# Performance work log

Hardware: AMD Instinct MI355X
Metric: run time of the kernel (lower is better)

## Reference

```python
import jax, jax.numpy as jnp
import numpy as np

B, C, L = 8, 256, 8192
H, D = 8, 64
INNER = H * D


def setup_inputs() -> dict:
    key = jax.random.key(0)
    ks = jax.random.split(key, 6)
    scale = 1.0 / np.sqrt(C)
    x = jax.random.normal(ks[0], (B, C, L), dtype=jnp.float32)
    Wq = jax.random.normal(ks[1], (INNER, C), dtype=jnp.float32) * scale
    Wk = jax.random.normal(ks[2], (INNER, C), dtype=jnp.float32) * scale
    Wv = jax.random.normal(ks[3], (INNER, C), dtype=jnp.float32) * scale
    Wo = jax.random.normal(ks[4], (C, INNER), dtype=jnp.float32) * (1.0 / np.sqrt(INNER))
    bo = jax.random.normal(ks[5], (C,), dtype=jnp.float32) * 0.01
    return {"x": x, "Wq": Wq, "Wk": Wk, "Wv": Wv, "Wo": Wo, "bo": bo}


def reference(x, Wq, Wk, Wv, Wo, bo):
    # 1x1 Conv1d == per-position matmul over channels: (inner,C) x (B,C,L) -> (B,inner,L)
    def proj(W):
        y = jnp.einsum('ic,bcl->bil', W, x)          # (B, inner, L)
        return y.reshape(B, H, D, L).transpose(0, 1, 3, 2)  # (B, H, L, D)

    q = jax.nn.softmax(proj(Wq), axis=-1)   # softmax over feature dim d
    k = jax.nn.softmax(proj(Wk), axis=-2)   # softmax over length dim L
    v = proj(Wv)

    context = jnp.einsum('bhld,bhlm->bhdm', k, v)   # (B, H, D, D)
    out = jnp.einsum('bhld,bhdm->bhlm', q, context) # (B, H, L, D)
    out = out.transpose(0, 1, 3, 2).reshape(B, INNER, L)  # (B, inner, L)
    return jnp.einsum('ci,bil->bcl', Wo, out) + bo[None, :, None]
```

## Files before the change

### kernel.cpp

```cpp
#include <hip/hip_runtime.h>

#define Bn 8
#define Cn 256
#define Ln 8192
#define Hn 8
#define Dn 64
#define IN 512
#define NSLAB 32

typedef __attribute__((ext_vector_type(4))) float f32x4;
typedef __attribute__((ext_vector_type(8))) __bf16 bf16x8;
typedef __attribute__((ext_vector_type(8))) unsigned short us8;

__device__ __forceinline__ float bf2f(unsigned short u) {
  unsigned int i = ((unsigned int)u) << 16;
  return __builtin_bit_cast(float, i);
}
__device__ __forceinline__ unsigned short f2bf(float f) {
  unsigned int i = __builtin_bit_cast(unsigned int, f);
  i += 0x7FFFu + ((i >> 16) & 1u);
  return (unsigned short)(i >> 16);
}
__device__ __forceinline__ bf16x8 asbf(us8 u) { return __builtin_bit_cast(bf16x8, u); }
__device__ __forceinline__ f32x4 mfma16(bf16x8 a, bf16x8 b, f32x4 c) {
  return __builtin_amdgcn_mfma_f32_16x16x32_bf16(a, b, c, 0, 0, 0);
}
__device__ __forceinline__ void gll16(const void* g, void* l) {
  __builtin_amdgcn_global_load_lds((const __attribute__((address_space(1))) void*)g,
                                   (__attribute__((address_space(3))) void*)l, 16, 0, 0);
}

__global__ __launch_bounds__(256) void k_xt(const float* __restrict__ x,
                                            unsigned short* __restrict__ xT) {
  __shared__ unsigned short tl[64 * 66];
  const int t = threadIdx.x;
  const int l0 = blockIdx.x * 64, c0 = blockIdx.y * 64, b = blockIdx.z;
#pragma unroll
  for (int it = 0; it < 4; ++it) {
    int lin = it * 256 + t;
    int c = lin >> 4;
    int l4 = (lin & 15) * 4;
    const float* gp = x + ((size_t)(b * Cn + c0 + c) * Ln + l0 + l4);
    f32x4 v = *(const f32x4*)gp;
    unsigned int p0 = (unsigned int)f2bf(v[0]) | ((unsigned int)f2bf(v[1]) << 16);
    unsigned int p1 = (unsigned int)f2bf(v[2]) | ((unsigned int)f2bf(v[3]) << 16);
    unsigned int* d = (unsigned int*)&tl[c * 66 + l4];
    d[0] = p0;
    d[1] = p1;
  }
  __syncthreads();
#pragma unroll
  for (int it = 0; it < 2; ++it) {
    int lin = it * 256 + t;
    int l = lin >> 3;
    int s = lin & 7;
    unsigned short v[8];
#pragma unroll
    for (int j = 0; j < 8; ++j) v[j] = tl[(s * 8 + j) * 66 + l];
    uint4 pk;
    pk.x = (unsigned)v[0] | ((unsigned)v[1] << 16);
    pk.y = (unsigned)v[2] | ((unsigned)v[3] << 16);
    pk.z = (unsigned)v[4] | ((unsigned)v[5] << 16);
    pk.w = (unsigned)v[6] | ((unsigned)v[7] << 16);
    *(uint4*)&xT[(size_t)(b * Ln + l0 + l) * Cn + c0 + s * 8] = pk;
  }
}

__global__ __launch_bounds__(256) void k_wcv(const float* __restrict__ Wq, const float* __restrict__ Wk,
                                             const float* __restrict__ Wv, const float* __restrict__ Wo,
                                             unsigned short* __restrict__ Wqkv,
                                             unsigned short* __restrict__ Wob) {
  int i = (blockIdx.x * 256 + threadIdx.x) * 4;
  const float* s;
  unsigned short* d;
  if (i < 393216) {
    int p = i >> 17;
    int w = i & 131071;
    s = (p == 0 ? Wq : (p == 1 ? Wk : Wv)) + w;
    d = Wqkv + i;
  } else {
    int w = i - 393216;
    s = Wo + w;
    d = Wob + w;
  }
  f32x4 v = *(const f32x4*)s;
  uint2 pk;
  pk.x = (unsigned)f2bf(v[0]) | ((unsigned)f2bf(v[1]) << 16);
  pk.y = (unsigned)f2bf(v[2]) | ((unsigned)f2bf(v[3]) << 16);
  *(uint2*)d = pk;
}

__global__ __launch_bounds__(256) void k_projq(const unsigned short* __restrict__ xT,
                                               const unsigned short* __restrict__ Wqkv,
                                               unsigned short* __restrict__ SqT) {
  __shared__ unsigned short lds[18432];
  const int tid = threadIdx.x, lane = tid & 63, wave = tid >> 6;
  const int lr = lane & 15, lg = lane >> 4;
  const int n0 = blockIdx.x * 128, m0 = blockIdx.y * 128, b = blockIdx.z;
  const int wm = (wave >> 1) * 64, wn = (wave & 1) * 64;
  unsigned short* Wt = lds;
  unsigned short* Xt = lds + 8192;

  f32x4 zero = {0.f, 0.f, 0.f, 0.f};
  f32x4 acc[4][4];
#pragma unroll
  for (int mt = 0; mt < 4; ++mt)
#pragma unroll
    for (int nt = 0; nt < 4; ++nt) acc[mt][nt] = zero;

  const int sr = tid >> 3, sc = (tid & 7) * 8;
  const unsigned short* wsrc = Wqkv + (size_t)(m0 + sr) * Cn + sc;
  const unsigned short* xsrc = xT + (size_t)(b * Ln + n0 + sr) * Cn + sc;

  for (int kt = 0; kt < 4; ++kt) {
    const int k0 = kt * 64;
#pragma unroll
    for (int it = 0; it < 4; ++it) {
      gll16(wsrc + (size_t)(it * 32) * Cn + k0, Wt + it * 2048 + tid * 8);
      gll16(xsrc + (size_t)(it * 32) * Cn + k0, Xt + it * 2048 + tid * 8);
    }
    __syncthreads();
#pragma unroll
    for (int ks = 0; ks < 2; ++ks) {
      const int kc = ks * 32 + lg * 8;
      bf16x8 af[4], bfv[4];
#pragma unroll
      for (int mt = 0; mt < 4; ++mt)
        af[mt] = asbf(*(const us8*)(Wt + (wm + mt * 16 + lr) * 64 + kc));
#pragma unroll
      for (int nt = 0; nt < 4; ++nt)
        bfv[nt] = asbf(*(const us8*)(Xt + (wn + nt * 16 + lr) * 64 + kc));
#pragma unroll
      for (int mt = 0; mt < 4; ++mt)
#pragma unroll
        for (int nt = 0; nt < 4; ++nt) acc[mt][nt] = mfma16(af[mt], bfv[nt], acc[mt][nt]);
    }
    __syncthreads();
  }

  unsigned short* T = lds + wave * 4608;
#pragma unroll
  for (int mt = 0; mt < 4; ++mt)
#pragma unroll
    for (int nt = 0; nt < 4; ++nt) {
      int ll = nt * 16 + lr, ii = mt * 16 + lg * 4;
      uint2 pk;
      pk.x = (unsigned)f2bf(acc[mt][nt][0]) | ((unsigned)f2bf(acc[mt][nt][1]) << 16);
      pk.y = (unsigned)f2bf(acc[mt][nt][2]) | ((unsigned)f2bf(acc[mt][nt][3]) << 16);
      *(uint2*)&T[ll * 72 + ii] = pk;
    }
  __syncthreads();
#pragma unroll
  for (int p = 0; p < 8; ++p) {
    int ll = p * 8 + (lane >> 3), s = lane & 7;
    uint4 v = *(const uint4*)&T[ll * 72 + s * 8];
    *(uint4*)&SqT[(size_t)(b * Ln + n0 + wn + ll) * IN + m0 + wm + s * 8] = v;
  }
}

__global__ __launch_bounds__(256) void k_projkv(const unsigned short* __restrict__ xT,
                                                const unsigned short* __restrict__ Wqkv,
                                                float* __restrict__ ctxP,
                                                float* __restrict__ den) {
  __shared__ unsigned short lds[17408];
  unsigned short* Wt = lds;
  unsigned short* Xt = lds + 8192;
  unsigned short* ek = lds;
  unsigned short* vt = lds + 64 * 136;
  const int tid = threadIdx.x, lane = tid & 63, wave = tid >> 6;
  const int lr = lane & 15, lg = lane >> 4;
  const int h = blockIdx.y, b = blockIdx.z;
  const int l0 = blockIdx.x * 256;
  const int wm = (wave >> 1) * 64, wn = (wave & 1) * 64;
  const int sr = tid >> 3, sc = (tid & 7) * 8;
  f32x4 zero = {0.f, 0.f, 0.f, 0.f};

  f32x4 cacc[4];
  cacc[0] = zero; cacc[1] = zero; cacc[2] = zero; cacc[3] = zero;
  float dacc[4][4] = {};

  for (int sub = 0; sub < 2; ++sub) {
    const int ls = l0 + sub * 128;
    f32x4 acc[4][4];
#pragma unroll
    for (int mt = 0; mt < 4; ++mt)
#pragma unroll
      for (int nt = 0; nt < 4; ++nt) acc[mt][nt] = zero;

    const unsigned short* xsrc = xT + (size_t)(b * Ln + ls + sr) * Cn + sc;
    for (int kt = 0; kt < 4; ++kt) {
      const int k0 = kt * 64;
#pragma unroll
      for (int it = 0; it < 4; ++it) {
        int gr = (it < 2 ? 512 : 960) + h * 64 + it * 32 + sr;
        gll16(Wqkv + (size_t)gr * Cn + k0 + sc, Wt + it * 2048 + tid * 8);
        gll16(xsrc + (size_t)(it * 32) * Cn + k0, Xt + it * 2048 + tid * 8);
      }
      __syncthreads();
#pragma unroll
      for (int ks = 0; ks < 2; ++ks) {
        const int kc = ks * 32 + lg * 8;
        bf16x8 af[4], bfv[4];
#pragma unroll
        for (int mt = 0; mt < 4; ++mt)
          af[mt] = asbf(*(const us8*)(Wt + (wm + mt * 16 + lr) * 64 + kc));
#pragma unroll
        for (int nt = 0; nt < 4; ++nt)
          bfv[nt] = asbf(*(const us8*)(Xt + (wn + nt * 16 + lr) * 64 + kc));
#pragma unroll
        for (int mt = 0; mt < 4; ++mt)
#pragma unroll
          for (int nt = 0; nt < 4; ++nt) acc[mt][nt] = mfma16(af[mt], bfv[nt], acc[mt][nt]);
      }
      __syncthreads();
    }

    if (wave < 2) {
#pragma unroll
      for (int mt = 0; mt < 4; ++mt)
#pragma unroll
        for (int nt = 0; nt < 4; ++nt) {
          int lcol = wn + nt * 16 + lr;
#pragma unroll
          for (int r = 0; r < 4; ++r) {
            float e = __expf(acc[mt][nt][r]);
            dacc[mt][r] += e;
            ek[(mt * 16 + lg * 4 + r) * 136 + lcol] = f2bf(e);
          }
        }
    } else {
#pragma unroll
      for (int mt = 0; mt < 4; ++mt)
#pragma unroll
        for (int nt = 0; nt < 4; ++nt) {
          int lcol = wn + nt * 16 + lr;
#pragma unroll
          for (int r = 0; r < 4; ++r)
            vt[(mt * 16 + lg * 4 + r) * 136 + lcol] = f2bf(acc[mt][nt][r]);
        }
    }
    __syncthreads();

    const int mq = wave * 16;
#pragma unroll
    for (int ks = 0; ks < 4; ++ks) {
      const int kc = ks * 32 + lg * 8;
      bf16x8 a = asbf(*(const us8*)(vt + (mq + lr) * 136 + kc));
#pragma unroll
      for (int dt = 0; dt < 4; ++dt) {
        bf16x8 bb = asbf(*(const us8*)(ek + (dt * 16 + lr) * 136 + kc));
        cacc[dt] = mfma16(a, bb, cacc[dt]);
      }
    }
    __syncthreads();
  }

  if (wave < 2) {
#pragma unroll
    for (int mt = 0; mt < 4; ++mt)
#pragma unroll
      for (int r = 0; r < 4; ++r) {
        float v = dacc[mt][r];
        v += __shfl_xor(v, 1);
        v += __shfl_xor(v, 2);
        v += __shfl_xor(v, 4);
        v += __shfl_xor(v, 8);
        if (lr == 0) atomicAdd(&den[(b * Hn + h) * 64 + mt * 16 + lg * 4 + r], v);
      }
  }
  float* cb = ctxP + ((size_t)blockIdx.x * 64 + b * Hn + h) * 4096;
  const int mq = wave * 16;
#pragma unroll
  for (int dt = 0; dt < 4; ++dt)
#pragma unroll
    for (int r = 0; r < 4; ++r)
      cb[(mq + lg * 4 + r) * 64 + dt * 16 + lr] = cacc[dt][r];
}

__global__ __launch_bounds__(256) void k_nrm(const float* __restrict__ ctxP,
                                             const float* __restrict__ den,
                                             unsigned short* __restrict__ ctxb) {
  const int bh = blockIdx.x, mz = blockIdx.y, t = threadIdx.x;
  const int m = mz * 16 + (t >> 4), dc = (t & 15) * 4;
  const float* base = ctxP + (size_t)bh * 4096 + m * 64 + dc;
  f32x4 s = {0.f, 0.f, 0.f, 0.f};
  for (int sl = 0; sl < NSLAB; ++sl) {
    f32x4 v = *(const f32x4*)(base + (size_t)sl * 64 * 4096);
    s += v;
  }
  f32x4 d4 = *(const f32x4*)(den + bh * 64 + dc);
  uint2 pk;
  pk.x = (unsigned)f2bf(s[0] / d4[0]) | ((unsigned)f2bf(s[1] / d4[1]) << 16);
  pk.y = (unsigned)f2bf(s[2] / d4[2]) | ((unsigned)f2bf(s[3] / d4[3]) << 16);
  *(uint2*)(ctxb + (size_t)bh * 4096 + m * 64 + dc) = pk;
}

__global__ __launch_bounds__(256) void k_out(const unsigned short* __restrict__ SqT,
                                             const unsigned short* __restrict__ ctxb,
                                             const unsigned short* __restrict__ Wob,
                                             const float* __restrict__ bo,
                                             float* __restrict__ out) {
  __shared__ unsigned short ot[64 * 256];
  const int tid = threadIdx.x, lane = tid & 63, w = tid >> 6;
  const int lr = lane & 15, lg = lane >> 4;
  const int l0 = blockIdx.x * 64, b = blockIdx.y;
  f32x4 zero = {0.f, 0.f, 0.f, 0.f};

  f32x4 acc[4][4];
#pragma unroll
  for (int mt = 0; mt < 4; ++mt)
#pragma unroll
    for (int nt = 0; nt < 4; ++nt) acc[mt][nt] = zero;

  const unsigned short* qb = SqT + (size_t)(b * Ln + l0 + w * 16 + lr) * IN + lg * 8;
  us8 r0 = *(const us8*)qb;
  us8 r1 = *(const us8*)(qb + 32);
  for (int half = 0; half < 2; ++half) {
#pragma unroll
    for (int hh = 0; hh < 4; ++hh) {
      const int h = half * 4 + hh;
      us8 n0, n1;
      if (h < 7) {
        n0 = *(const us8*)(qb + (h + 1) * 64);
        n1 = *(const us8*)(qb + (h + 1) * 64 + 32);
      }
      float qv[16];
#pragma unroll
      for (int j = 0; j < 8; ++j) {
        qv[j] = bf2f(r0[j]);
        qv[8 + j] = bf2f(r1[j]);
      }
      float mx = qv[0];
#pragma unroll
      for (int j = 1; j < 16; ++j) mx = fmaxf(mx, qv[j]);
      mx = fmaxf(mx, __shfl_xor(mx, 16));
      mx = fmaxf(mx, __shfl_xor(mx, 32));
      float sm = 0.f;
#pragma unroll
      for (int j = 0; j < 16; ++j) {
        qv[j] = __expf(qv[j] - mx);
        sm += qv[j];
      }
      sm += __shfl_xor(sm, 16);
      sm += __shfl_xor(sm, 32);
      float rs = 1.0f / sm;
      us8 a0u, a1u;
#pragma unroll
      for (int j = 0; j < 8; ++j) {
        a0u[j] = f2bf(qv[j] * rs);
        a1u[j] = f2bf(qv[8 + j] * rs);
      }
      bf16x8 a0 = asbf(a0u), a1 = asbf(a1u);
      const unsigned short* cbb = ctxb + (size_t)(b * Hn + h) * 4096;
#pragma unroll
      for (int mt = 0; mt < 4; ++mt) {
        bf16x8 bu0 = asbf(*(const us8*)(cbb + (mt * 16 + lr) * 64 + lg * 8));
        bf16x8 bu1 = asbf(*(const us8*)(cbb + (mt * 16 + lr) * 64 + 32 + lg * 8));
        f32x4 oa = mfma16(a0, bu0, zero);
        oa = mfma16(a1, bu1, oa);
        int ib = hh * 64 + mt * 16 + lr;
#pragma unroll
        for (int r = 0; r < 4; ++r) {
          int ll = w * 16 + lg * 4 + r;
          ot[(ll * 256 + ib) ^ ((ll & 7) << 3)] = f2bf(oa[r]);
        }
      }
      r0 = n0;
      r1 = n1;
    }
    __syncthreads();

    const unsigned short* wB = Wob + (size_t)(w * 64 + lr) * IN + half * 256;
#pragma unroll 2
    for (int ks = 0; ks < 8; ++ks) {
      int kc = ks * 32 + lg * 8;
      bf16x8 af[4], bf4[4];
#pragma unroll
      for (int mt = 0; mt < 4; ++mt) af[mt] = asbf(*(const us8*)(wB + mt * 16 * IN + kc));
#pragma unroll
      for (int nt = 0; nt < 4; ++nt) {
        int ll = nt * 16 + lr;
        bf4[nt] = asbf(*(const us8*)&ot[(ll * 256 + kc) ^ ((ll & 7) << 3)]);
      }
#pragma unroll
      for (int mt = 0; mt < 4; ++mt)
#pragma unroll
        for (int nt = 0; nt < 4; ++nt) acc[mt][nt] = mfma16(af[mt], bf4[nt], acc[mt][nt]);
    }
    __syncthreads();
  }
#pragma unroll
  for (int mt = 0; mt < 4; ++mt) {
    int c = w * 64 + mt * 16 + lg * 4;
#pragma unroll
    for (int r = 0; r < 4; ++r) {
      float bb = bo[c + r];
      float* op = out + (size_t)(b * Cn + c + r) * Ln + l0;
#pragma unroll
      for (int nt = 0; nt < 4; ++nt) op[nt * 16 + lr] = acc[mt][nt][r] + bb;
    }
  }
}

extern "C" void kernel_launch(void* const* d_in, const int* in_sizes, int n_in,
                              void* d_out, int out_size, void* d_ws, size_t ws_size,
                              hipStream_t stream) {
  const float* x = (const float*)d_in[0];
  const float* Wq = (const float*)d_in[1];
  const float* Wk = (const float*)d_in[2];
  const float* Wv = (const float*)d_in[3];
  const float* Wo = (const float*)d_in[4];
  const float* bo = (const float*)d_in[5];
  float* out = (float*)d_out;

  char* ws = (char*)d_ws;
  size_t o = 0;
  unsigned short* xT = (unsigned short*)(ws + o);   o += (size_t)Bn * Ln * Cn * 2;
  unsigned short* Wqkv = (unsigned short*)(ws + o); o += (size_t)1536 * Cn * 2;
  unsigned short* Wob = (unsigned short*)(ws + o);  o += (size_t)Cn * IN * 2;
  unsigned short* SqT = (unsigned short*)(ws + o);  o += (size_t)Bn * Ln * IN * 2;
  float* ctxP = (float*)(ws + o);                   o += (size_t)NSLAB * 64 * 4096 * 4;
  float* den = (float*)(ws + o);                    o += (size_t)Bn * Hn * 64 * 4;
  unsigned short* ctxb = (unsigned short*)(ws + o); o += (size_t)Bn * Hn * 64 * 64 * 2;

  hipMemsetAsync(den, 0, (size_t)Bn * Hn * 64 * 4, stream);
  k_xt<<<dim3(Ln / 64, Cn / 64, Bn), 256, 0, stream>>>(x, xT);
  k_wcv<<<512, 256, 0, stream>>>(Wq, Wk, Wv, Wo, Wqkv, Wob);
  k_projq<<<dim3(Ln / 128, 4, Bn), 256, 0, stream>>>(xT, Wqkv, SqT);
  k_projkv<<<dim3(Ln / 256, Hn, Bn), 256, 0, stream>>>(xT, Wqkv, ctxP, den);
  k_nrm<<<dim3(Bn * Hn, 4), 256, 0, stream>>>(ctxP, den, ctxb);
  k_out<<<dim3(Ln / 64, Bn), 256, 0, stream>>>(SqT, ctxb, Wob, bo, out);
}
```

Measured before the change: 317.4 us.

## Fold context into output weights and fuse q softmax into projection

The q softmax moves into the q projection epilogue, so the stored activations are already normalized. The per-head context is folded into Wo ahead of time, producing a per-batch (C x inner) weight. The output stage then becomes a plain tiled GEMM over q instead of a per-head context matmul through LDS followed by the Wo matmul. The kv projection also covers 512 positions per block, which halves the partial-context slabs that need reducing. This adds a small fold kernel and a per-batch folded-weight buffer, and the folded weights are rounded to bf16, which slightly changes precision.

After: 271.8 us. 14.4% less time.

```diff
diff --git a/kernel.cpp b/kernel.cpp
--- a/kernel.cpp
+++ b/kernel.cpp
@@ -6,7 +6,7 @@
 #define Hn 8
 #define Dn 64
 #define IN 512
-#define NSLAB 32
+#define NSLAB 16
 
 typedef __attribute__((ext_vector_type(4))) float f32x4;
 typedef __attribute__((ext_vector_type(8))) __bf16 bf16x8;
@@ -90,9 +90,9 @@
   *(uint2*)d = pk;
 }
 
-__global__ __launch_bounds__(256) void k_projq(const unsigned short* __restrict__ xT,
-                                               const unsigned short* __restrict__ Wqkv,
-                                               unsigned short* __restrict__ SqT) {
+__global__ __launch_bounds__(256) void k_qs(const unsigned short* __restrict__ xT,
+                                            const unsigned short* __restrict__ Wqkv,
+                                            unsigned short* __restrict__ qhT) {
   __shared__ unsigned short lds[18432];
   const int tid = threadIdx.x, lane = tid & 63, wave = tid >> 6;
   const int lr = lane & 15, lg = lane >> 4;
@@ -140,21 +140,41 @@
 
   unsigned short* T = lds + wave * 4608;
 #pragma unroll
-  for (int mt = 0; mt < 4; ++mt)
-#pragma unroll
-    for (int nt = 0; nt < 4; ++nt) {
-      int ll = nt * 16 + lr, ii = mt * 16 + lg * 4;
+  for (int nt = 0; nt < 4; ++nt) {
+    float qv[16];
+#pragma unroll
+    for (int mt = 0; mt < 4; ++mt)
+#pragma unroll
+      for (int r = 0; r < 4; ++r) qv[mt * 4 + r] = acc[mt][nt][r];
+    float mx = qv[0];
+#pragma unroll
+    for (int j = 1; j < 16; ++j) mx = fmaxf(mx, qv[j]);
+    mx = fmaxf(mx, __shfl_xor(mx, 16));
+    mx = fmaxf(mx, __shfl_xor(mx, 32));
+    float sm = 0.f;
+#pragma unroll
+    for (int j = 0; j < 16; ++j) {
+      qv[j] = __expf(qv[j] - mx);
+      sm += qv[j];
+    }
+    sm += __shfl_xor(sm, 16);
+    sm += __shfl_xor(sm, 32);
+    float rs = 1.0f / sm;
+    int ll = nt * 16 + lr;
+#pragma unroll
+    for (int mt = 0; mt < 4; ++mt) {
       uint2 pk;
-      pk.x = (unsigned)f2bf(acc[mt][nt][0]) | ((unsigned)f2bf(acc[mt][nt][1]) << 16);
-      pk.y = (unsigned)f2bf(acc[mt][nt][2]) | ((unsigned)f2bf(acc[mt][nt][3]) << 16);
-      *(uint2*)&T[ll * 72 + ii] = pk;
-    }
+      pk.x = (unsigned)f2bf(qv[mt * 4 + 0] * rs) | ((unsigned)f2bf(qv[mt * 4 + 1] * rs) << 16);
+      pk.y = (unsigned)f2bf(qv[mt * 4 + 2] * rs) | ((unsigned)f2bf(qv[mt * 4 + 3] * rs) << 16);
+      *(uint2*)&T[ll * 72 + mt * 16 + lg * 4] = pk;
+    }
+  }
   __syncthreads();
 #pragma unroll
   for (int p = 0; p < 8; ++p) {
     int ll = p * 8 + (lane >> 3), s = lane & 7;
     uint4 v = *(const uint4*)&T[ll * 72 + s * 8];
-    *(uint4*)&SqT[(size_t)(b * Ln + n0 + wn + ll) * IN + m0 + wm + s * 8] = v;
+    *(uint4*)&qhT[(size_t)(b * Ln + n0 + wn + ll) * IN + m0 + wm + s * 8] = v;
   }
 }
 
@@ -170,7 +190,7 @@
   const int tid = threadIdx.x, lane = tid & 63, wave = tid >> 6;
   const int lr = lane & 15, lg = lane >> 4;
   const int h = blockIdx.y, b = blockIdx.z;
-  const int l0 = blockIdx.x * 256;
+  const int l0 = blockIdx.x * 512;
   const int wm = (wave >> 1) * 64, wn = (wave & 1) * 64;
   const int sr = tid >> 3, sc = (tid & 7) * 8;
   f32x4 zero = {0.f, 0.f, 0.f, 0.f};
@@ -179,7 +199,7 @@
   cacc[0] = zero; cacc[1] = zero; cacc[2] = zero; cacc[3] = zero;
   float dacc[4][4] = {};
 
-  for (int sub = 0; sub < 2; ++sub) {
+  for (int sub = 0; sub < 4; ++sub) {
     const int ls = l0 + sub * 128;
     f32x4 acc[4][4];
 #pragma unroll
@@ -279,123 +299,121 @@
 
 __global__ __launch_bounds__(256) void k_nrm(const float* __restrict__ ctxP,
                                              const float* __restrict__ den,
-                                             unsigned short* __restrict__ ctxb) {
-  const int bh = blockIdx.x, mz = blockIdx.y, t = threadIdx.x;
-  const int m = mz * 16 + (t >> 4), dc = (t & 15) * 4;
-  const float* base = ctxP + (size_t)bh * 4096 + m * 64 + dc;
-  f32x4 s = {0.f, 0.f, 0.f, 0.f};
-  for (int sl = 0; sl < NSLAB; ++sl) {
-    f32x4 v = *(const f32x4*)(base + (size_t)sl * 64 * 4096);
-    s += v;
-  }
-  f32x4 d4 = *(const f32x4*)(den + bh * 64 + dc);
-  uint2 pk;
-  pk.x = (unsigned)f2bf(s[0] / d4[0]) | ((unsigned)f2bf(s[1] / d4[1]) << 16);
-  pk.y = (unsigned)f2bf(s[2] / d4[2]) | ((unsigned)f2bf(s[3] / d4[3]) << 16);
-  *(uint2*)(ctxb + (size_t)bh * 4096 + m * 64 + dc) = pk;
-}
-
-__global__ __launch_bounds__(256) void k_out(const unsigned short* __restrict__ SqT,
-                                             const unsigned short* __restrict__ ctxb,
-                                             const unsigned short* __restrict__ Wob,
-                                             const float* __restrict__ bo,
-                                             float* __restrict__ out) {
-  __shared__ unsigned short ot[64 * 256];
-  const int tid = threadIdx.x, lane = tid & 63, w = tid >> 6;
+                                             unsigned short* __restrict__ ctxdm) {
+  const int bh = blockIdx.x, t = threadIdx.x;
+  const int m = t >> 2, dq = (t & 3) * 16;
+  const float* base = ctxP + (size_t)bh * 4096 + m * 64 + dq;
+  const float* dnb = den + bh * 64 + dq;
+#pragma unroll
+  for (int q = 0; q < 4; ++q) {
+    f32x4 s = {0.f, 0.f, 0.f, 0.f};
+    for (int sl = 0; sl < NSLAB; ++sl) s += *(const f32x4*)(base + (size_t)sl * 64 * 4096 + q * 4);
+    f32x4 d4 = *(const f32x4*)(dnb + q * 4);
+#pragma unroll
+    for (int j = 0; j < 4; ++j)
+      ctxdm[(size_t)bh * 4096 + (dq + q * 4 + j) * 64 + m] = f2bf(s[j] / d4[j]);
+  }
+}
+
+__global__ __launch_bounds__(256) void k_fold(const unsigned short* __restrict__ Wob,
+                                              const unsigned short* __restrict__ ctxdm,
+                                              unsigned short* __restrict__ Wfold) {
+  const int tid = threadIdx.x, lane = tid & 63, wave = tid >> 6;
   const int lr = lane & 15, lg = lane >> 4;
-  const int l0 = blockIdx.x * 64, b = blockIdx.y;
+  const int h = blockIdx.x, b = blockIdx.y;
+  const int c0 = wave * 64;
   f32x4 zero = {0.f, 0.f, 0.f, 0.f};
-
   f32x4 acc[4][4];
 #pragma unroll
   for (int mt = 0; mt < 4; ++mt)
 #pragma unroll
     for (int nt = 0; nt < 4; ++nt) acc[mt][nt] = zero;
-
-  const unsigned short* qb = SqT + (size_t)(b * Ln + l0 + w * 16 + lr) * IN + lg * 8;
-  us8 r0 = *(const us8*)qb;
-  us8 r1 = *(const us8*)(qb + 32);
-  for (int half = 0; half < 2; ++half) {
-#pragma unroll
-    for (int hh = 0; hh < 4; ++hh) {
-      const int h = half * 4 + hh;
-      us8 n0, n1;
-      if (h < 7) {
-        n0 = *(const us8*)(qb + (h + 1) * 64);
-        n1 = *(const us8*)(qb + (h + 1) * 64 + 32);
-      }
-      float qv[16];
-#pragma unroll
-      for (int j = 0; j < 8; ++j) {
-        qv[j] = bf2f(r0[j]);
-        qv[8 + j] = bf2f(r1[j]);
-      }
-      float mx = qv[0];
-#pragma unroll
-      for (int j = 1; j < 16; ++j) mx = fmaxf(mx, qv[j]);
-      mx = fmaxf(mx, __shfl_xor(mx, 16));
-      mx = fmaxf(mx, __shfl_xor(mx, 32));
-      float sm = 0.f;
-#pragma unroll
-      for (int j = 0; j < 16; ++j) {
-        qv[j] = __expf(qv[j] - mx);
-        sm += qv[j];
-      }
-      sm += __shfl_xor(sm, 16);
-      sm += __shfl_xor(sm, 32);
-      float rs = 1.0f / sm;
-      us8 a0u, a1u;
-#pragma unroll
-      for (int j = 0; j < 8; ++j) {
-        a0u[j] = f2bf(qv[j] * rs);
-        a1u[j] = f2bf(qv[8 + j] * rs);
-      }
-      bf16x8 a0 = asbf(a0u), a1 = asbf(a1u);
-      const unsigned short* cbb = ctxb + (size_t)(b * Hn + h) * 4096;
-#pragma unroll
-      for (int mt = 0; mt < 4; ++mt) {
-        bf16x8 bu0 = asbf(*(const us8*)(cbb + (mt * 16 + lr) * 64 + lg * 8));
-        bf16x8 bu1 = asbf(*(const us8*)(cbb + (mt * 16 + lr) * 64 + 32 + lg * 8));
-        f32x4 oa = mfma16(a0, bu0, zero);
-        oa = mfma16(a1, bu1, oa);
-        int ib = hh * 64 + mt * 16 + lr;
-#pragma unroll
-        for (int r = 0; r < 4; ++r) {
-          int ll = w * 16 + lg * 4 + r;
-          ot[(ll * 256 + ib) ^ ((ll & 7) << 3)] = f2bf(oa[r]);
-        }
-      }
-      r0 = n0;
-      r1 = n1;
-    }
-    __syncthreads();
-
-    const unsigned short* wB = Wob + (size_t)(w * 64 + lr) * IN + half * 256;
-#pragma unroll 2
-    for (int ks = 0; ks < 8; ++ks) {
-      int kc = ks * 32 + lg * 8;
-      bf16x8 af[4], bf4[4];
-#pragma unroll
-      for (int mt = 0; mt < 4; ++mt) af[mt] = asbf(*(const us8*)(wB + mt * 16 * IN + kc));
-#pragma unroll
-      for (int nt = 0; nt < 4; ++nt) {
-        int ll = nt * 16 + lr;
-        bf4[nt] = asbf(*(const us8*)&ot[(ll * 256 + kc) ^ ((ll & 7) << 3)]);
-      }
-#pragma unroll
-      for (int mt = 0; mt < 4; ++mt)
-#pragma unroll
-        for (int nt = 0; nt < 4; ++nt) acc[mt][nt] = mfma16(af[mt], bf4[nt], acc[mt][nt]);
-    }
-    __syncthreads();
-  }
+  const unsigned short* cdb = ctxdm + (size_t)(b * Hn + h) * 4096;
+#pragma unroll
+  for (int ks = 0; ks < 2; ++ks) {
+    const int kc = ks * 32 + lg * 8;
+    bf16x8 af[4], bf4[4];
+#pragma unroll
+    for (int mt = 0; mt < 4; ++mt)
+      af[mt] = asbf(*(const us8*)(Wob + (size_t)(c0 + mt * 16 + lr) * IN + h * 64 + kc));
+#pragma unroll
+    for (int nt = 0; nt < 4; ++nt)
+      bf4[nt] = asbf(*(const us8*)(cdb + (nt * 16 + lr) * 64 + kc));
+#pragma unroll
+    for (int mt = 0; mt < 4; ++mt)
+#pragma unroll
+      for (int nt = 0; nt < 4; ++nt) acc[mt][nt] = mfma16(af[mt], bf4[nt], acc[mt][nt]);
+  }
+  unsigned short* wf = Wfold + (size_t)b * Cn * IN;
+#pragma unroll
+  for (int mt = 0; mt < 4; ++mt)
+#pragma unroll
+    for (int nt = 0; nt < 4; ++nt) {
+      int c = c0 + mt * 16 + lg * 4;
+      int d = h * 64 + nt * 16 + lr;
+#pragma unroll
+      for (int r = 0; r < 4; ++r) wf[(size_t)(c + r) * IN + d] = f2bf(acc[mt][nt][r]);
+    }
+}
+
+__global__ __launch_bounds__(256) void k_wo(const unsigned short* __restrict__ qhT,
+                                            const unsigned short* __restrict__ Wfold,
+                                            const float* __restrict__ bo,
+                                            float* __restrict__ out) {
+  __shared__ unsigned short lds[16384];
+  const int tid = threadIdx.x, lane = tid & 63, wave = tid >> 6;
+  const int lr = lane & 15, lg = lane >> 4;
+  const int gl = blockIdx.x * 128;
+  const int b = gl >> 13, l0 = gl & 8191;
+  const int m0 = blockIdx.y * 128;
+  const int wm = (wave >> 1) * 64, wn = (wave & 1) * 64;
+  unsigned short* Wt = lds;
+  unsigned short* Qt = lds + 8192;
+
+  f32x4 zero = {0.f, 0.f, 0.f, 0.f};
+  f32x4 acc[4][4];
+#pragma unroll
+  for (int mt = 0; mt < 4; ++mt)
+#pragma unroll
+    for (int nt = 0; nt < 4; ++nt) acc[mt][nt] = zero;
+
+  const int sr = tid >> 3, sc = (tid & 7) * 8;
+  const unsigned short* wsrc = Wfold + (size_t)b * Cn * IN + (size_t)(m0 + sr) * IN + sc;
+  const unsigned short* qsrc = qhT + (size_t)(b * Ln + l0 + sr) * IN + sc;
+
+  for (int kt = 0; kt < 8; ++kt) {
+    const int k0 = kt * 64;
+#pragma unroll
+    for (int it = 0; it < 4; ++it) {
+      gll16(wsrc + (size_t)(it * 32) * IN + k0, Wt + it * 2048 + tid * 8);
+      gll16(qsrc + (size_t)(it * 32) * IN + k0, Qt + it * 2048 + tid * 8);
+    }
+    __syncthreads();
+#pragma unroll
+    for (int ks = 0; ks < 2; ++ks) {
+      const int kc = ks * 32 + lg * 8;
+      bf16x8 af[4], bfv[4];
+#pragma unroll
+      for (int mt = 0; mt < 4; ++mt)
+        af[mt] = asbf(*(const us8*)(Wt + (wm + mt * 16 + lr) * 64 + kc));
+#pragma unroll
+      for (int nt = 0; nt < 4; ++nt)
+        bfv[nt] = asbf(*(const us8*)(Qt + (wn + nt * 16 + lr) * 64 + kc));
+#pragma unroll
+      for (int mt = 0; mt < 4; ++mt)
+#pragma unroll
+        for (int nt = 0; nt < 4; ++nt) acc[mt][nt] = mfma16(af[mt], bfv[nt], acc[mt][nt]);
+    }
+    __syncthreads();
+  }
+
 #pragma unroll
   for (int mt = 0; mt < 4; ++mt) {
-    int c = w * 64 + mt * 16 + lg * 4;
+    int c = m0 + wm + mt * 16 + lg * 4;
 #pragma unroll
     for (int r = 0; r < 4; ++r) {
       float bb = bo[c + r];
-      float* op = out + (size_t)(b * Cn + c + r) * Ln + l0;
+      float* op = out + (size_t)(b * Cn + c + r) * Ln + l0 + wn;
 #pragma unroll
       for (int nt = 0; nt < 4; ++nt) op[nt * 16 + lr] = acc[mt][nt][r] + bb;
     }
@@ -415,19 +433,21 @@
 
   char* ws = (char*)d_ws;
   size_t o = 0;
-  unsigned short* xT = (unsigned short*)(ws + o);   o += (size_t)Bn * Ln * Cn * 2;
-  unsigned short* Wqkv = (unsigned short*)(ws + o); o += (size_t)1536 * Cn * 2;
-  unsigned short* Wob = (unsigned short*)(ws + o);  o += (size_t)Cn * IN * 2;
-  unsigned short* SqT = (unsigned short*)(ws + o);  o += (size_t)Bn * Ln * IN * 2;
-  float* ctxP = (float*)(ws + o);                   o += (size_t)NSLAB * 64 * 4096 * 4;
-  float* den = (float*)(ws + o);                    o += (size_t)Bn * Hn * 64 * 4;
-  unsigned short* ctxb = (unsigned short*)(ws + o); o += (size_t)Bn * Hn * 64 * 64 * 2;
+  unsigned short* xT = (unsigned short*)(ws + o);    o += (size_t)Bn * Ln * Cn * 2;
+  unsigned short* Wqkv = (unsigned short*)(ws + o);  o += (size_t)1536 * Cn * 2;
+  unsigned short* Wob = (unsigned short*)(ws + o);   o += (size_t)Cn * IN * 2;
+  unsigned short* qhT = (unsigned short*)(ws + o);   o += (size_t)Bn * Ln * IN * 2;
+  float* ctxP = (float*)(ws + o);                    o += (size_t)NSLAB * 64 * 4096 * 4;
+  float* den = (float*)(ws + o);                     o += (size_t)Bn * Hn * 64 * 4;
+  unsigned short* ctxdm = (unsigned short*)(ws + o); o += (size_t)Bn * Hn * 64 * 64 * 2;
+  unsigned short* Wfold = (unsigned short*)(ws + o); o += (size_t)Bn * Cn * IN * 2;
 
   hipMemsetAsync(den, 0, (size_t)Bn * Hn * 64 * 4, stream);
   k_xt<<<dim3(Ln / 64, Cn / 64, Bn), 256, 0, stream>>>(x, xT);
   k_wcv<<<512, 256, 0, stream>>>(Wq, Wk, Wv, Wo, Wqkv, Wob);
-  k_projq<<<dim3(Ln / 128, 4, Bn), 256, 0, stream>>>(xT, Wqkv, SqT);
-  k_projkv<<<dim3(Ln / 256, Hn, Bn), 256, 0, stream>>>(xT, Wqkv, ctxP, den);
-  k_nrm<<<dim3(Bn * Hn, 4), 256, 0, stream>>>(ctxP, den, ctxb);
-  k_out<<<dim3(Ln / 64, Bn), 256, 0, stream>>>(SqT, ctxb, Wob, bo, out);
-}
+  k_qs<<<dim3(Ln / 128, 4, Bn), 256, 0, stream>>>(xT, Wqkv, qhT);
+  k_projkv<<<dim3(Ln / 512, Hn, Bn), 256, 0, stream>>>(xT, Wqkv, ctxP, den);
+  k_nrm<<<Bn * Hn, 256, 0, stream>>>(ctxP, den, ctxdm);
+  k_fold<<<dim3(Hn, Bn), 256, 0, stream>>>(Wob, ctxdm, Wfold);
+  k_wo<<<dim3(Bn * Ln / 128, 2), 256, 0, stream>>>(qhT, Wfold, bo, out);
+}
```
